# Kernel tuning notes

Hardware: AMD Instinct MI355X
Metric: run time of the kernel (lower is better)

## Reference

```python
import jax, jax.numpy as jnp
import numpy as np

EPS_RMS = 1e-6
EPS_Q = 1e-5


def rmsnorm(x, g):
    var = jnp.mean(x * x, axis=-1, keepdims=True)
    return g * (x * jax.lax.rsqrt(var + EPS_RMS))


def activation_quant(x):
    # per-token 8-bit fake quant with straight-through estimator
    scale = 127.0 / jnp.clip(jnp.max(jnp.abs(x), axis=-1, keepdims=True), EPS_Q)
    y = jnp.clip(jnp.round(x * scale), -128, 127) / scale
    return x + jax.lax.stop_gradient(y - x)


def weight_quant(w):
    # per-tensor ternary fake quant with straight-through estimator
    s = jnp.clip(jnp.mean(jnp.abs(w)), EPS_Q)
    y = jnp.clip(jnp.round(w / s), -1, 1) * s
    return w + jax.lax.stop_gradient(y - w)


def bitlinear(x, w, g):
    xq = activation_quant(rmsnorm(x, g))
    wq = weight_quant(w)
    return jnp.einsum('btc,oc->bto', xq, wq)


def setup_inputs() -> dict:
    key = jax.random.key(0)
    ks = jax.random.split(key, 5)
    B, T, C = 2, 2048, 1024
    std = 1.0 / np.sqrt(C)
    inp = {
        'x': jax.random.normal(ks[0], (B, T, C), jnp.float32),
        'wq': jax.random.normal(ks[1], (C, C), jnp.float32) * std,
        'wk': jax.random.normal(ks[2], (C, C), jnp.float32) * std,
        'wv': jax.random.normal(ks[3], (C, C), jnp.float32) * std,
        'wo': jax.random.normal(ks[4], (C, C), jnp.float32) * std,
        'gq': jnp.ones((C,), jnp.float32),
        'gk': jnp.ones((C,), jnp.float32),
        'gv': jnp.ones((C,), jnp.float32),
        'go': jnp.ones((C,), jnp.float32),
    }
    return inp


def reference(x, wq, wk, wv, wo, gq, gk, gv, go):
    B, T, C = x.shape
    n_head = 16
    head_dim = C // n_head

    q = bitlinear(x, wq, gq).reshape(B, T, n_head, head_dim).transpose(0, 2, 1, 3)
    k = bitlinear(x, wk, gk).reshape(B, T, n_head, head_dim).transpose(0, 2, 1, 3)
    v = bitlinear(x, wv, gv).reshape(B, T, n_head, head_dim).transpose(0, 2, 1, 3)

    att = jnp.einsum('bhqd,bhkd->bhqk', q, k) * (1.0 / np.sqrt(head_dim))
    causal = jnp.tril(jnp.ones((T, T), dtype=bool))  # [T,T]
    att = jnp.where(causal[None, None], att, -jnp.inf)
    att = jax.nn.softmax(att, axis=-1)

    y = jnp.einsum('bhqk,bhkd->bhqd', att, v)
    y = y.transpose(0, 2, 1, 3).reshape(B, T, C)
    return bitlinear(y, wo, go)
```

## Files before the change

kernel.cpp:

```cpp
#include <hip/hip_runtime.h>
#include <hip/hip_bf16.h>


typedef __attribute__((ext_vector_type(8))) short bf16x8;
typedef __attribute__((ext_vector_type(4))) float f32x4;
typedef __attribute__((ext_vector_type(4))) int i32x4;

__device__ __forceinline__ f32x4 mfma16(bf16x8 a, bf16x8 b, f32x4 c) {
    return __builtin_amdgcn_mfma_f32_16x16x32_bf16(a, b, c, 0, 0, 0);
}

__device__ __forceinline__ i32x4 mfma_i8(i32x4 a, i32x4 b, i32x4 c) {
    return __builtin_amdgcn_mfma_i32_16x16x64_i8(a, b, c, 0, 0, 0);
}

__device__ __forceinline__ unsigned short f2bf(float f) {
    unsigned int u = __float_as_uint(f);
    unsigned int r = (u + 0x7fffu + ((u >> 16) & 1u)) >> 16;
    return (unsigned short)r;
}

__device__ __forceinline__ unsigned int cvtpk_bf16(float lo, float hi) {
    unsigned int r;
    asm("v_cvt_pk_bf16_f32 %0, %1, %2" : "=v"(r) : "v"(lo), "v"(hi));
    return r;
}

__device__ __forceinline__ float exp2_fast(float x) {
    float r;
    asm("v_exp_f32 %0, %1" : "=v"(r) : "v"(x));
    return r;
}

__device__ __forceinline__ void gload_lds16(const void* g, void* l) {
    __builtin_amdgcn_global_load_lds((const __attribute__((address_space(1))) unsigned int*)g,
                                     (__attribute__((address_space(3))) unsigned int*)l, 16, 0, 0);
}

__device__ __forceinline__ int pack4i8(float a, float b, float c, float d) {
    unsigned int u = ((unsigned int)((int)a & 255)) | (((unsigned int)((int)b & 255)) << 8) |
                     (((unsigned int)((int)c & 255)) << 16) | (((unsigned int)((int)d & 255)) << 24);
    return (int)u;
}

__device__ __forceinline__ float wredsum(float v) {
#pragma unroll
    for (int o = 32; o > 0; o >>= 1) v += __shfl_xor(v, o);
    return v;
}
__device__ __forceinline__ float wredmax(float v) {
#pragma unroll
    for (int o = 32; o > 0; o >>= 1) v = fmaxf(v, __shfl_xor(v, o));
    return v;
}

__global__ __launch_bounds__(256) void wabssum(const float* __restrict__ w0, const float* __restrict__ w1,
                                               const float* __restrict__ w2, const float* __restrict__ w3,
                                               float* __restrict__ part) {
    int widx = blockIdx.x >> 5, b = blockIdx.x & 31;
    const float* w = (widx == 0) ? w0 : (widx == 1) ? w1 : (widx == 2) ? w2 : w3;
    const float4* w4 = (const float4*)w;
    int tid = threadIdx.x;
    float s = 0.f;
    int base = b * 8192 + tid;
#pragma unroll
    for (int i = 0; i < 32; ++i) {
        float4 v = w4[base + i * 256];
        s += fabsf(v.x) + fabsf(v.y) + fabsf(v.z) + fabsf(v.w);
    }
    s = wredsum(s);
    __shared__ float red[4];
    int wid = tid >> 6, lid = tid & 63;
    if (lid == 0) red[wid] = s;
    __syncthreads();
    if (tid == 0) part[blockIdx.x] = red[0] + red[1] + red[2] + red[3];
}

__global__ __launch_bounds__(256) void wquant(const float* __restrict__ w0, const float* __restrict__ w1,
                                              const float* __restrict__ w2, const float* __restrict__ w3,
                                              const float* __restrict__ part, signed char* __restrict__ wq8) {
    int widx = blockIdx.x >> 6, b = blockIdx.x & 63;
    const float* w = (widx == 0) ? w0 : (widx == 1) ? w1 : (widx == 2) ? w2 : w3;
    float s = 0.f;
#pragma unroll
    for (int i = 0; i < 32; ++i) s += part[widx * 32 + i];
    s = fmaxf(s * (1.f / 1048576.f), 1e-5f);
    float inv = 1.f / s;
    const float4* w4 = (const float4*)w;
    int* dst = (int*)(wq8 + (size_t)widx * 1048576);
    int tid = threadIdx.x;
#pragma unroll
    for (int it = 0; it < 16; ++it) {
        int i4 = b * 4096 + it * 256 + tid;
        float4 v = w4[i4];
        float q0 = fminf(fmaxf(rintf(v.x * inv), -1.f), 1.f);
        float q1 = fminf(fmaxf(rintf(v.y * inv), -1.f), 1.f);
        float q2 = fminf(fmaxf(rintf(v.z * inv), -1.f), 1.f);
        float q3 = fminf(fmaxf(rintf(v.w * inv), -1.f), 1.f);
        dst[i4] = pack4i8(q0, q1, q2, q3);
    }
}

template <int NP>
__global__ __launch_bounds__(256) void actquant(const float* __restrict__ x, const float* __restrict__ g0,
                                                const float* __restrict__ g1, const float* __restrict__ g2,
                                                signed char* __restrict__ aq, float* __restrict__ ascale) {
    int m = blockIdx.x, tid = threadIdx.x;
    int wid = tid >> 6, lid = tid & 63;
    __shared__ float red[4];
    float4 xv = ((const float4*)(x + (size_t)m * 1024))[tid];
    float ss = xv.x * xv.x + xv.y * xv.y + xv.z * xv.z + xv.w * xv.w;
    ss = wredsum(ss);
    if (lid == 0) red[wid] = ss;
    __syncthreads();
    float rstd = rsqrtf((red[0] + red[1] + red[2] + red[3]) * (1.f / 1024.f) + 1e-6f);
    const float* gs[3] = {g0, g1, g2};
#pragma unroll
    for (int p = 0; p < NP; ++p) {
        float4 gv = ((const float4*)gs[p])[tid];
        float a0 = xv.x * gv.x * rstd, a1 = xv.y * gv.y * rstd;
        float a2 = xv.z * gv.z * rstd, a3 = xv.w * gv.w * rstd;
        float am = fmaxf(fmaxf(fabsf(a0), fabsf(a1)), fmaxf(fabsf(a2), fabsf(a3)));
        am = wredmax(am);
        __syncthreads();
        if (lid == 0) red[wid] = am;
        __syncthreads();
        float rm = fmaxf(fmaxf(red[0], red[1]), fmaxf(red[2], red[3]));
        float scale = 127.f / fmaxf(rm, 1e-5f);
        float q0 = fminf(fmaxf(rintf(a0 * scale), -128.f), 127.f);
        float q1 = fminf(fmaxf(rintf(a1 * scale), -128.f), 127.f);
        float q2 = fminf(fmaxf(rintf(a2 * scale), -128.f), 127.f);
        float q3 = fminf(fmaxf(rintf(a3 * scale), -128.f), 127.f);
        ((int*)(aq + (size_t)p * 4194304 + (size_t)m * 1024))[tid] = pack4i8(q0, q1, q2, q3);
        if (tid == 0) ascale[p * 4096 + m] = scale;
    }
}

template <int MODE>
__device__ __forceinline__ void gemm_core(const signed char* __restrict__ A,
                                          const float* __restrict__ asc,
                                          const signed char* __restrict__ W, float s_w,
                                          void* __restrict__ outp, int bm, int bn,
                                          char* As, char* Bs) {
    int tid = threadIdx.x;
    int w = tid >> 6, l = tid & 63;
    int wr = w >> 1, wc = w & 1;
    int lr = l & 15, lh = l >> 4;
    i32x4 acc[4][4] = {};
    int srow = l >> 3;
    int scolb = (((l & 7) ^ srow)) * 16;
    int key16 = (lr & 7) * 16;
    const signed char* Ab = A + (size_t)(bm * 128) * 1024;
    const signed char* Wb = W + (size_t)(bn * 128) * 1024;

    auto STAGE = [&](int kt, int buf) {
        int k0 = kt * 128;
        char* Ad = As + buf * 16384;
        char* Bd = Bs + buf * 16384;
#pragma unroll
        for (int j = 0; j < 4; ++j) {
            int c = j * 4 + w;
            gload_lds16(Ab + (size_t)(c * 8 + srow) * 1024 + k0 + scolb, Ad + c * 1024);
            gload_lds16(Wb + (size_t)(c * 8 + srow) * 1024 + k0 + scolb, Bd + c * 1024);
        }
    };

    STAGE(0, 0);
    __syncthreads();
    for (int kt = 0; kt < 8; ++kt) {
        int cur = kt & 1;
        if (kt < 7) STAGE(kt + 1, cur ^ 1);
        const char* Ar = As + cur * 16384;
        const char* Br = Bs + cur * 16384;
#pragma unroll
        for (int ks = 0; ks < 2; ++ks) {
            int kb = (ks * 64 + lh * 16) ^ key16;
            i32x4 af[4], bfr[4];
#pragma unroll
            for (int mi = 0; mi < 4; ++mi) af[mi] = *(const i32x4*)&Ar[(wr * 64 + mi * 16 + lr) * 128 + kb];
#pragma unroll
            for (int ni = 0; ni < 4; ++ni) bfr[ni] = *(const i32x4*)&Br[(wc * 64 + ni * 16 + lr) * 128 + kb];
#pragma unroll
            for (int mi = 0; mi < 4; ++mi)
#pragma unroll
                for (int ni = 0; ni < 4; ++ni) acc[mi][ni] = mfma_i8(af[mi], bfr[ni], acc[mi][ni]);
        }
        __syncthreads();
    }
#pragma unroll
    for (int mi = 0; mi < 4; ++mi) {
        int mbase = bm * 128 + wr * 64 + mi * 16 + lh * 4;
#pragma unroll
        for (int ni = 0; ni < 4; ++ni) {
            int n = bn * 128 + wc * 64 + ni * 16 + lr;
            if (MODE == 1) {
                int b = mbase >> 11, t0 = mbase & 2047;
                int h = n >> 6, d = n & 63;
                ushort4 st;
                st.x = f2bf((float)acc[mi][ni][0] * s_w / asc[mbase + 0]);
                st.y = f2bf((float)acc[mi][ni][1] * s_w / asc[mbase + 1]);
                st.z = f2bf((float)acc[mi][ni][2] * s_w / asc[mbase + 2]);
                st.w = f2bf((float)acc[mi][ni][3] * s_w / asc[mbase + 3]);
                *(ushort4*)&((unsigned short*)outp)[(size_t)(b * 16 + h) * 131072 + (size_t)d * 2048 + t0] = st;
            } else {
#pragma unroll
                for (int i = 0; i < 4; ++i) {
                    int m = mbase + i;
                    float val = (float)acc[mi][ni][i] * s_w / asc[m];
                    if (MODE == 0) {
                        int b = m >> 11, t = m & 2047, h = n >> 6, d = n & 63;
                        ((unsigned short*)outp)[(size_t)(b * 16 + h) * 131072 + (size_t)t * 64 + d] = f2bf(val);
                    } else {
                        ((float*)outp)[(size_t)m * 1024 + n] = val;
                    }
                }
            }
        }
    }
}

__device__ __forceinline__ float sw_from_part(const float* part) {
    float s = 0.f;
#pragma unroll
    for (int i = 0; i < 32; ++i) s += part[i];
    return fmaxf(s * (1.f / 1048576.f), 1e-5f);
}

__global__ __launch_bounds__(256) void gemm_qkv(const signed char* __restrict__ abf,
                                                const float* __restrict__ ascale,
                                                const signed char* __restrict__ wq8,
                                                const float* __restrict__ part,
                                                unsigned short* __restrict__ qbf,
                                                unsigned short* __restrict__ kbf,
                                                unsigned short* __restrict__ vtb) {
    __shared__ alignas(16) char As[32768];
    __shared__ alignas(16) char Bs[32768];
    int z = blockIdx.z;
    const signed char* A = abf + (size_t)z * 4194304;
    const float* asc = ascale + z * 4096;
    const signed char* W = wq8 + (size_t)z * 1048576;
    float s_w = sw_from_part(part + z * 32);
    int bm = blockIdx.x, bn = blockIdx.y;
    if (z == 0) {
        gemm_core<0>(A, asc, W, s_w, qbf, bm, bn, As, Bs);
    } else if (z == 1) {
        gemm_core<0>(A, asc, W, s_w, kbf, bm, bn, As, Bs);
    } else {
        gemm_core<1>(A, asc, W, s_w, vtb, bm, bn, As, Bs);
    }
}

__global__ __launch_bounds__(256) void gemm_o(const signed char* __restrict__ A,
                                              const float* __restrict__ asc,
                                              const signed char* __restrict__ W,
                                              const float* __restrict__ part, float* __restrict__ outp) {
    __shared__ alignas(16) char As[32768];
    __shared__ alignas(16) char Bs[32768];
    float s_w = sw_from_part(part);
    gemm_core<2>(A, asc, W, s_w, outp, blockIdx.x, blockIdx.y, As, Bs);
}

__global__ __launch_bounds__(64) void attn(const unsigned short* __restrict__ qb,
                                           const unsigned short* __restrict__ kb,
                                           const unsigned short* __restrict__ vt, float* __restrict__ y) {
    int blk = blockIdx.x;
    int bh = blk & 31;
    int c = 63 - (blk >> 5);
    int q0 = c << 5;
    int l = threadIdx.x & 63;
    int lr = l & 15, lh = l >> 4;
    const unsigned short* qbase = qb + (size_t)bh * 131072;
    const unsigned short* kbase = kb + (size_t)bh * 131072;
    const unsigned short* vbase = vt + (size_t)bh * 131072;

    bf16x8 qf00 = *(const bf16x8*)&qbase[(size_t)(q0 + lr) * 64 + lh * 8];
    bf16x8 qf01 = *(const bf16x8*)&qbase[(size_t)(q0 + lr) * 64 + 32 + lh * 8];
    bf16x8 qf10 = *(const bf16x8*)&qbase[(size_t)(q0 + 16 + lr) * 64 + lh * 8];
    bf16x8 qf11 = *(const bf16x8*)&qbase[(size_t)(q0 + 16 + lr) * 64 + 32 + lh * 8];

    f32x4 o[4][2] = {};
    const float ninf = -__builtin_inff();
    const float SC = 0.125f * 1.44269504f;
    float mreg0 = ninf, mreg1 = ninf;
    float lreg0 = 0.f, lreg1 = 0.f;
    __shared__ alignas(16) unsigned short plds[2][16][40];

    int qrow0 = q0 + lr, qrow1 = q0 + 16 + lr;
    int ntiles = c + 1;

    auto LOADK = [&](int kv0, bf16x8* k) {
        k[0] = *(const bf16x8*)&kbase[(size_t)(kv0 + lr) * 64 + lh * 8];
        k[1] = *(const bf16x8*)&kbase[(size_t)(kv0 + lr) * 64 + 32 + lh * 8];
        k[2] = *(const bf16x8*)&kbase[(size_t)(kv0 + 16 + lr) * 64 + lh * 8];
        k[3] = *(const bf16x8*)&kbase[(size_t)(kv0 + 16 + lr) * 64 + 32 + lh * 8];
    };
    auto LOADV = [&](int kv0, bf16x8* v) {
        v[0] = *(const bf16x8*)&vbase[(size_t)(lr)*2048 + kv0 + lh * 8];
        v[1] = *(const bf16x8*)&vbase[(size_t)(16 + lr) * 2048 + kv0 + lh * 8];
        v[2] = *(const bf16x8*)&vbase[(size_t)(32 + lr) * 2048 + kv0 + lh * 8];
        v[3] = *(const bf16x8*)&vbase[(size_t)(48 + lr) * 2048 + kv0 + lh * 8];
    };
    auto PROCESS = [&](int t, bf16x8* k, bf16x8* v) {
        int kv0 = t << 5;
        __builtin_amdgcn_s_setprio(1);
        f32x4 s00 = {}, s01 = {}, s10 = {}, s11 = {};
        s00 = mfma16(k[0], qf00, s00);
        s00 = mfma16(k[1], qf01, s00);
        s01 = mfma16(k[2], qf00, s01);
        s01 = mfma16(k[3], qf01, s01);
        s10 = mfma16(k[0], qf10, s10);
        s10 = mfma16(k[1], qf11, s10);
        s11 = mfma16(k[2], qf10, s11);
        s11 = mfma16(k[3], qf11, s11);
        __builtin_amdgcn_s_setprio(0);
        float p0[8], p1[8];
        if (t == c) {
#pragma unroll
            for (int r = 0; r < 4; ++r) {
                int kva = kv0 + lh * 4 + r, kvb = kv0 + 16 + lh * 4 + r;
                p0[r]     = (kva <= qrow0) ? s00[r] * SC : ninf;
                p0[r + 4] = (kvb <= qrow0) ? s01[r] * SC : ninf;
                p1[r]     = (kva <= qrow1) ? s10[r] * SC : ninf;
                p1[r + 4] = (kvb <= qrow1) ? s11[r] * SC : ninf;
            }
        } else {
#pragma unroll
            for (int r = 0; r < 4; ++r) {
                p0[r] = s00[r] * SC;
                p0[r + 4] = s01[r] * SC;
                p1[r] = s10[r] * SC;
                p1[r + 4] = s11[r] * SC;
            }
        }
        float t0 = fmaxf(fmaxf(fmaxf(p0[0], p0[1]), fmaxf(p0[2], p0[3])),
                         fmaxf(fmaxf(p0[4], p0[5]), fmaxf(p0[6], p0[7])));
        float t1 = fmaxf(fmaxf(fmaxf(p1[0], p1[1]), fmaxf(p1[2], p1[3])),
                         fmaxf(fmaxf(p1[4], p1[5]), fmaxf(p1[6], p1[7])));
        t0 = fmaxf(t0, __shfl_xor(t0, 16));
        t0 = fmaxf(t0, __shfl_xor(t0, 32));
        t1 = fmaxf(t1, __shfl_xor(t1, 16));
        t1 = fmaxf(t1, __shfl_xor(t1, 32));
        if (__any((t0 > mreg0 + 11.f) || (t1 > mreg1 + 11.f))) {
            float mn0 = fmaxf(mreg0, t0), mn1 = fmaxf(mreg1, t1);
            float cc0 = exp2_fast(mreg0 - mn0), cc1 = exp2_fast(mreg1 - mn1);
            lreg0 *= cc0;
            lreg1 *= cc1;
            mreg0 = mn0;
            mreg1 = mn1;
#pragma unroll
            for (int dt = 0; dt < 4; ++dt)
#pragma unroll
                for (int r = 0; r < 4; ++r) {
                    o[dt][0][r] *= cc0;
                    o[dt][1][r] *= cc1;
                }
        }
        float ps0[8], ps1[8];
#pragma unroll
        for (int r = 0; r < 8; ++r) {
            ps0[r] = exp2_fast(p0[r] - mreg0);
            ps1[r] = exp2_fast(p1[r] - mreg1);
        }
        float sum0 = ((ps0[0] + ps0[1]) + (ps0[2] + ps0[3])) + ((ps0[4] + ps0[5]) + (ps0[6] + ps0[7]));
        float sum1 = ((ps1[0] + ps1[1]) + (ps1[2] + ps1[3])) + ((ps1[4] + ps1[5]) + (ps1[6] + ps1[7]));
        sum0 += __shfl_xor(sum0, 16);
        sum0 += __shfl_xor(sum0, 32);
        sum1 += __shfl_xor(sum1, 16);
        sum1 += __shfl_xor(sum1, 32);
        lreg0 += sum0;
        lreg1 += sum1;
        uint2 w0lo, w0hi, w1lo, w1hi;
        w0lo.x = cvtpk_bf16(ps0[0], ps0[1]);
        w0lo.y = cvtpk_bf16(ps0[2], ps0[3]);
        w0hi.x = cvtpk_bf16(ps0[4], ps0[5]);
        w0hi.y = cvtpk_bf16(ps0[6], ps0[7]);
        w1lo.x = cvtpk_bf16(ps1[0], ps1[1]);
        w1lo.y = cvtpk_bf16(ps1[2], ps1[3]);
        w1hi.x = cvtpk_bf16(ps1[4], ps1[5]);
        w1hi.y = cvtpk_bf16(ps1[6], ps1[7]);
        *(uint2*)&plds[0][lr][lh * 4] = w0lo;
        *(uint2*)&plds[0][lr][16 + lh * 4] = w0hi;
        *(uint2*)&plds[1][lr][lh * 4] = w1lo;
        *(uint2*)&plds[1][lr][16 + lh * 4] = w1hi;
        bf16x8 pf0 = *(const bf16x8*)&plds[0][lr][lh * 8];
        bf16x8 pf1 = *(const bf16x8*)&plds[1][lr][lh * 8];
        __builtin_amdgcn_s_setprio(1);
#pragma unroll
        for (int dt = 0; dt < 4; ++dt) {
            o[dt][0] = mfma16(v[dt], pf0, o[dt][0]);
            o[dt][1] = mfma16(v[dt], pf1, o[dt][1]);
        }
        __builtin_amdgcn_s_setprio(0);
    };

    bf16x8 kA[4], vA[4], kB[4], vB[4];
    LOADK(0, kA);
    LOADV(0, vA);
    int t = 0;
    while (true) {
        if (t + 1 < ntiles) { LOADK((t + 1) << 5, kB); LOADV((t + 1) << 5, vB); }
        PROCESS(t, kA, vA);
        if (++t >= ntiles) break;
        if (t + 1 < ntiles) { LOADK((t + 1) << 5, kA); LOADV((t + 1) << 5, vA); }
        PROCESS(t, kB, vB);
        if (++t >= ntiles) break;
    }

    int b = bh >> 4, h = bh & 15;
#pragma unroll
    for (int qt = 0; qt < 2; ++qt) {
        int qrow = (qt == 0) ? qrow0 : qrow1;
        float invl = 1.f / ((qt == 0) ? lreg0 : lreg1);
        float* yr = y + (size_t)(b * 2048 + qrow) * 1024 + h * 64;
#pragma unroll
        for (int dt = 0; dt < 4; ++dt) {
            float4 st;
            st.x = o[dt][qt][0] * invl;
            st.y = o[dt][qt][1] * invl;
            st.z = o[dt][qt][2] * invl;
            st.w = o[dt][qt][3] * invl;
            *(float4*)&yr[dt * 16 + lh * 4] = st;
        }
    }
}

extern "C" void kernel_launch(void* const* d_in, const int* in_sizes, int n_in,
                              void* d_out, int out_size, void* d_ws, size_t ws_size,
                              hipStream_t stream) {
    const float* x  = (const float*)d_in[0];
    const float* wq = (const float*)d_in[1];
    const float* wk = (const float*)d_in[2];
    const float* wv = (const float*)d_in[3];
    const float* wo = (const float*)d_in[4];
    const float* gq = (const float*)d_in[5];
    const float* gk = (const float*)d_in[6];
    const float* gv = (const float*)d_in[7];
    const float* go = (const float*)d_in[8];

    char* ws = (char*)d_ws;
    size_t off = 0;
    auto alloc = [&](size_t bytes) {
        size_t o = off;
        off += (bytes + 255) & ~(size_t)255;
        return o;
    };
    float* part = (float*)(ws + alloc(128 * 4));
    signed char* wq8 = (signed char*)(ws + alloc(4ull * 1048576));
    signed char* abf = (signed char*)(ws + alloc(3ull * 4194304));
    float* asc = (float*)(ws + alloc(3ull * 4096 * 4));
    unsigned short* qbf = (unsigned short*)(ws + alloc(4194304ull * 2));
    unsigned short* kbf = (unsigned short*)(ws + alloc(4194304ull * 2));
    unsigned short* vtb = (unsigned short*)(ws + alloc(4194304ull * 2));
    float* ybuf = (float*)(ws + alloc(4194304ull * 4));
    signed char* ybf = (signed char*)(ws + alloc(4194304ull));
    float* ysc = (float*)(ws + alloc(4096 * 4));
    (void)ws_size; (void)in_sizes; (void)n_in; (void)out_size;

    wabssum<<<128, 256, 0, stream>>>(wq, wk, wv, wo, part);
    wquant<<<256, 256, 0, stream>>>(wq, wk, wv, wo, part, wq8);
    actquant<3><<<4096, 256, 0, stream>>>(x, gq, gk, gv, abf, asc);
    gemm_qkv<<<dim3(32, 8, 3), 256, 0, stream>>>(abf, asc, wq8, part, qbf, kbf, vtb);
    attn<<<2048, 64, 0, stream>>>(qbf, kbf, vtb, ybuf);
    actquant<1><<<4096, 256, 0, stream>>>(ybuf, go, go, go, ybf, ysc);
    gemm_o<<<dim3(32, 8), 256, 0, stream>>>(ybf, ysc, wq8 + 3ull * 1048576, part + 96, (float*)d_out);
}
```

Baseline: 144.6 us.

## Split attention KV tiles across four waves with LDS merge of partial softmax

Each attention block now runs four wavefronts that take interleaved KV tiles (stride 4) for the same 32 query rows. Each wave keeps its own online-softmax state, and the partial outputs plus max/sum values are written to shared memory and combined in a log-sum-exp merge before the store. This shortens the serial KV loop per block, which was long for late query chunks and caused load imbalance and low occupancy. In exchange it adds about 32KB of LDS per block, a barrier, and merge arithmetic, and early query chunks leave some waves idle.

```diff
diff --git a/kernel.cpp b/kernel.cpp
--- a/kernel.cpp
+++ b/kernel.cpp
@@ -260,13 +260,14 @@
     gemm_core<2>(A, asc, W, s_w, outp, blockIdx.x, blockIdx.y, As, Bs);
 }
 
-__global__ __launch_bounds__(64) void attn(const unsigned short* __restrict__ qb,
-                                           const unsigned short* __restrict__ kb,
-                                           const unsigned short* __restrict__ vt, float* __restrict__ y) {
+__global__ __launch_bounds__(256) void attn(const unsigned short* __restrict__ qb,
+                                            const unsigned short* __restrict__ kb,
+                                            const unsigned short* __restrict__ vt, float* __restrict__ y) {
     int blk = blockIdx.x;
     int bh = blk & 31;
     int c = 63 - (blk >> 5);
     int q0 = c << 5;
+    int w = threadIdx.x >> 6;
     int l = threadIdx.x & 63;
     int lr = l & 15, lh = l >> 4;
     const unsigned short* qbase = qb + (size_t)bh * 131072;
@@ -283,10 +284,11 @@
     const float SC = 0.125f * 1.44269504f;
     float mreg0 = ninf, mreg1 = ninf;
     float lreg0 = 0.f, lreg1 = 0.f;
-    __shared__ alignas(16) unsigned short plds[2][16][40];
+    __shared__ alignas(16) unsigned short plds[4][2][16][40];
+    __shared__ alignas(16) float om[4][32][64];
+    __shared__ float mlm[4][2][32];
 
     int qrow0 = q0 + lr, qrow1 = q0 + 16 + lr;
-    int ntiles = c + 1;
 
     auto LOADK = [&](int kv0, bf16x8* k) {
         k[0] = *(const bf16x8*)&kbase[(size_t)(kv0 + lr) * 64 + lh * 8];
@@ -378,12 +380,12 @@
         w1lo.y = cvtpk_bf16(ps1[2], ps1[3]);
         w1hi.x = cvtpk_bf16(ps1[4], ps1[5]);
         w1hi.y = cvtpk_bf16(ps1[6], ps1[7]);
-        *(uint2*)&plds[0][lr][lh * 4] = w0lo;
-        *(uint2*)&plds[0][lr][16 + lh * 4] = w0hi;
-        *(uint2*)&plds[1][lr][lh * 4] = w1lo;
-        *(uint2*)&plds[1][lr][16 + lh * 4] = w1hi;
-        bf16x8 pf0 = *(const bf16x8*)&plds[0][lr][lh * 8];
-        bf16x8 pf1 = *(const bf16x8*)&plds[1][lr][lh * 8];
+        *(uint2*)&plds[w][0][lr][lh * 4] = w0lo;
+        *(uint2*)&plds[w][0][lr][16 + lh * 4] = w0hi;
+        *(uint2*)&plds[w][1][lr][lh * 4] = w1lo;
+        *(uint2*)&plds[w][1][lr][16 + lh * 4] = w1hi;
+        bf16x8 pf0 = *(const bf16x8*)&plds[w][0][lr][lh * 8];
+        bf16x8 pf1 = *(const bf16x8*)&plds[w][1][lr][lh * 8];
         __builtin_amdgcn_s_setprio(1);
 #pragma unroll
         for (int dt = 0; dt < 4; ++dt) {
@@ -393,34 +395,59 @@
         __builtin_amdgcn_s_setprio(0);
     };
 
-    bf16x8 kA[4], vA[4], kB[4], vB[4];
-    LOADK(0, kA);
-    LOADV(0, vA);
-    int t = 0;
-    while (true) {
-        if (t + 1 < ntiles) { LOADK((t + 1) << 5, kB); LOADV((t + 1) << 5, vB); }
-        PROCESS(t, kA, vA);
-        if (++t >= ntiles) break;
-        if (t + 1 < ntiles) { LOADK((t + 1) << 5, kA); LOADV((t + 1) << 5, vA); }
-        PROCESS(t, kB, vB);
-        if (++t >= ntiles) break;
-    }
-
+    int t = w;
+    if (t <= c) {
+        bf16x8 kA[4], vA[4], kB[4], vB[4];
+        LOADK(t << 5, kA);
+        LOADV(t << 5, vA);
+        while (true) {
+            if (t + 4 <= c) { LOADK((t + 4) << 5, kB); LOADV((t + 4) << 5, vB); }
+            PROCESS(t, kA, vA);
+            t += 4;
+            if (t > c) break;
+            if (t + 4 <= c) { LOADK((t + 4) << 5, kA); LOADV((t + 4) << 5, vA); }
+            PROCESS(t, kB, vB);
+            t += 4;
+            if (t > c) break;
+        }
+    }
+
+#pragma unroll
+    for (int dt = 0; dt < 4; ++dt) {
+        *(float4*)&om[w][lr][dt * 16 + lh * 4] = *(float4*)&o[dt][0];
+        *(float4*)&om[w][16 + lr][dt * 16 + lh * 4] = *(float4*)&o[dt][1];
+    }
+    if (lh == 0) {
+        mlm[w][0][lr] = mreg0;
+        mlm[w][1][lr] = lreg0;
+        mlm[w][0][16 + lr] = mreg1;
+        mlm[w][1][16 + lr] = lreg1;
+    }
+    __syncthreads();
+
+    int tid = threadIdx.x;
+    int row = tid >> 3;
+    int d0 = (tid & 7) * 8;
+    float m0 = mlm[0][0][row], m1 = mlm[1][0][row], m2 = mlm[2][0][row], m3 = mlm[3][0][row];
+    float ms = fmaxf(fmaxf(m0, m1), fmaxf(m2, m3));
+    float s0 = exp2_fast(m0 - ms), s1 = exp2_fast(m1 - ms);
+    float s2 = exp2_fast(m2 - ms), s3 = exp2_fast(m3 - ms);
+    float lt = mlm[0][1][row] * s0 + mlm[1][1][row] * s1 + mlm[2][1][row] * s2 + mlm[3][1][row] * s3;
+    float invl = 1.f / lt;
     int b = bh >> 4, h = bh & 15;
-#pragma unroll
-    for (int qt = 0; qt < 2; ++qt) {
-        int qrow = (qt == 0) ? qrow0 : qrow1;
-        float invl = 1.f / ((qt == 0) ? lreg0 : lreg1);
-        float* yr = y + (size_t)(b * 2048 + qrow) * 1024 + h * 64;
-#pragma unroll
-        for (int dt = 0; dt < 4; ++dt) {
-            float4 st;
-            st.x = o[dt][qt][0] * invl;
-            st.y = o[dt][qt][1] * invl;
-            st.z = o[dt][qt][2] * invl;
-            st.w = o[dt][qt][3] * invl;
-            *(float4*)&yr[dt * 16 + lh * 4] = st;
-        }
+    float* yr = y + (size_t)(b * 2048 + q0 + row) * 1024 + h * 64 + d0;
+#pragma unroll
+    for (int j = 0; j < 8; j += 4) {
+        float4 v0 = *(float4*)&om[0][row][d0 + j];
+        float4 v1 = *(float4*)&om[1][row][d0 + j];
+        float4 v2 = *(float4*)&om[2][row][d0 + j];
+        float4 v3 = *(float4*)&om[3][row][d0 + j];
+        float4 st;
+        st.x = (v0.x * s0 + v1.x * s1 + v2.x * s2 + v3.x * s3) * invl;
+        st.y = (v0.y * s0 + v1.y * s1 + v2.y * s2 + v3.y * s3) * invl;
+        st.z = (v0.z * s0 + v1.z * s1 + v2.z * s2 + v3.z * s3) * invl;
+        st.w = (v0.w * s0 + v1.w * s1 + v2.w * s2 + v3.w * s3) * invl;
+        *(float4*)&yr[j] = st;
     }
 }
 
@@ -460,7 +487,7 @@
     wquant<<<256, 256, 0, stream>>>(wq, wk, wv, wo, part, wq8);
     actquant<3><<<4096, 256, 0, stream>>>(x, gq, gk, gv, abf, asc);
     gemm_qkv<<<dim3(32, 8, 3), 256, 0, stream>>>(abf, asc, wq8, part, qbf, kbf, vtb);
-    attn<<<2048, 64, 0, stream>>>(qbf, kbf, vtb, ybuf);
+    attn<<<2048, 256, 0, stream>>>(qbf, kbf, vtb, ybuf);
     actquant<1><<<4096, 256, 0, stream>>>(ybuf, go, go, go, ybf, ysc);
     gemm_o<<<dim3(32, 8), 256, 0, stream>>>(ybf, ysc, wq8 + 3ull * 1048576, part + 96, (float*)d_out);
 }
```

Result: no change. 144.5 us (-0.1%).

## Share K/V tiles across four attention waves via swizzled LDS double buffering

Applied to the files above, without the earlier changes.

The attention kernel now runs four waves per block, each owning a 32-row query chunk of a 128-row group. K and V tiles are staged cooperatively into XOR-swizzled LDS with global-to-LDS loads and double-buffered, so each tile is fetched once per block instead of once per wave. This cuts global and L2 traffic but adds a __syncthreads per tile. Waves with fewer causal tiles sit idle until the block's last wave finishes, and the grid drops to 512 blocks.

```diff
diff --git a/kernel.cpp b/kernel.cpp
--- a/kernel.cpp
+++ b/kernel.cpp
@@ -260,18 +260,22 @@
     gemm_core<2>(A, asc, W, s_w, outp, blockIdx.x, blockIdx.y, As, Bs);
 }
 
-__global__ __launch_bounds__(64) void attn(const unsigned short* __restrict__ qb,
-                                           const unsigned short* __restrict__ kb,
-                                           const unsigned short* __restrict__ vt, float* __restrict__ y) {
+__global__ __launch_bounds__(256) void attn(const unsigned short* __restrict__ qb,
+                                            const unsigned short* __restrict__ kb,
+                                            const unsigned short* __restrict__ vt, float* __restrict__ y) {
     int blk = blockIdx.x;
     int bh = blk & 31;
-    int c = 63 - (blk >> 5);
-    int q0 = c << 5;
+    int g = 15 - (blk >> 5);
+    int w = threadIdx.x >> 6;
     int l = threadIdx.x & 63;
     int lr = l & 15, lh = l >> 4;
+    int cw = 4 * g + w;
+    int q0 = cw << 5;
+    int NT = 4 * g + 4;
+
     const unsigned short* qbase = qb + (size_t)bh * 131072;
-    const unsigned short* kbase = kb + (size_t)bh * 131072;
-    const unsigned short* vbase = vt + (size_t)bh * 131072;
+    const char* kbytes = (const char*)(kb + (size_t)bh * 131072);
+    const char* vbytes = (const char*)(vt + (size_t)bh * 131072);
 
     bf16x8 qf00 = *(const bf16x8*)&qbase[(size_t)(q0 + lr) * 64 + lh * 8];
     bf16x8 qf01 = *(const bf16x8*)&qbase[(size_t)(q0 + lr) * 64 + 32 + lh * 8];
@@ -283,38 +287,42 @@
     const float SC = 0.125f * 1.44269504f;
     float mreg0 = ninf, mreg1 = ninf;
     float lreg0 = 0.f, lreg1 = 0.f;
-    __shared__ alignas(16) unsigned short plds[2][16][40];
+
+    __shared__ alignas(16) char Ks[2][4096];
+    __shared__ alignas(16) char Vs[2][4096];
+    __shared__ alignas(16) unsigned short plds[4][2][16][40];
 
     int qrow0 = q0 + lr, qrow1 = q0 + 16 + lr;
-    int ntiles = c + 1;
-
-    auto LOADK = [&](int kv0, bf16x8* k) {
-        k[0] = *(const bf16x8*)&kbase[(size_t)(kv0 + lr) * 64 + lh * 8];
-        k[1] = *(const bf16x8*)&kbase[(size_t)(kv0 + lr) * 64 + 32 + lh * 8];
-        k[2] = *(const bf16x8*)&kbase[(size_t)(kv0 + 16 + lr) * 64 + lh * 8];
-        k[3] = *(const bf16x8*)&kbase[(size_t)(kv0 + 16 + lr) * 64 + 32 + lh * 8];
+
+    auto STAGE = [&](int t, int buf) {
+        int kv0 = t << 5;
+        gload_lds16(kbytes + (size_t)(kv0 + w * 8 + (l >> 3)) * 128 + (((l & 7) ^ (l >> 3)) * 16),
+                    &Ks[buf][w * 1024]);
+        gload_lds16(vbytes + (size_t)(w * 16 + (l >> 2)) * 4096 + (size_t)kv0 * 2 +
+                        (((l & 3) ^ ((l >> 2) & 3)) * 16),
+                    &Vs[buf][w * 1024]);
     };
-    auto LOADV = [&](int kv0, bf16x8* v) {
-        v[0] = *(const bf16x8*)&vbase[(size_t)(lr)*2048 + kv0 + lh * 8];
-        v[1] = *(const bf16x8*)&vbase[(size_t)(16 + lr) * 2048 + kv0 + lh * 8];
-        v[2] = *(const bf16x8*)&vbase[(size_t)(32 + lr) * 2048 + kv0 + lh * 8];
-        v[3] = *(const bf16x8*)&vbase[(size_t)(48 + lr) * 2048 + kv0 + lh * 8];
-    };
-    auto PROCESS = [&](int t, bf16x8* k, bf16x8* v) {
+
+    auto PROCESS = [&](int t, const char* Kb, const char* Vb) {
         int kv0 = t << 5;
+        int k7 = lr & 7;
+        bf16x8 k0 = *(const bf16x8*)(Kb + lr * 128 + ((lh ^ k7) * 16));
+        bf16x8 k1 = *(const bf16x8*)(Kb + lr * 128 + (((4 + lh) ^ k7) * 16));
+        bf16x8 k2 = *(const bf16x8*)(Kb + (16 + lr) * 128 + ((lh ^ k7) * 16));
+        bf16x8 k3 = *(const bf16x8*)(Kb + (16 + lr) * 128 + (((4 + lh) ^ k7) * 16));
         __builtin_amdgcn_s_setprio(1);
         f32x4 s00 = {}, s01 = {}, s10 = {}, s11 = {};
-        s00 = mfma16(k[0], qf00, s00);
-        s00 = mfma16(k[1], qf01, s00);
-        s01 = mfma16(k[2], qf00, s01);
-        s01 = mfma16(k[3], qf01, s01);
-        s10 = mfma16(k[0], qf10, s10);
-        s10 = mfma16(k[1], qf11, s10);
-        s11 = mfma16(k[2], qf10, s11);
-        s11 = mfma16(k[3], qf11, s11);
+        s00 = mfma16(k0, qf00, s00);
+        s00 = mfma16(k1, qf01, s00);
+        s01 = mfma16(k2, qf00, s01);
+        s01 = mfma16(k3, qf01, s01);
+        s10 = mfma16(k0, qf10, s10);
+        s10 = mfma16(k1, qf11, s10);
+        s11 = mfma16(k2, qf10, s11);
+        s11 = mfma16(k3, qf11, s11);
         __builtin_amdgcn_s_setprio(0);
         float p0[8], p1[8];
-        if (t == c) {
+        if (t == cw) {
 #pragma unroll
             for (int r = 0; r < 4; ++r) {
                 int kva = kv0 + lh * 4 + r, kvb = kv0 + 16 + lh * 4 + r;
@@ -378,32 +386,30 @@
         w1lo.y = cvtpk_bf16(ps1[2], ps1[3]);
         w1hi.x = cvtpk_bf16(ps1[4], ps1[5]);
         w1hi.y = cvtpk_bf16(ps1[6], ps1[7]);
-        *(uint2*)&plds[0][lr][lh * 4] = w0lo;
-        *(uint2*)&plds[0][lr][16 + lh * 4] = w0hi;
-        *(uint2*)&plds[1][lr][lh * 4] = w1lo;
-        *(uint2*)&plds[1][lr][16 + lh * 4] = w1hi;
-        bf16x8 pf0 = *(const bf16x8*)&plds[0][lr][lh * 8];
-        bf16x8 pf1 = *(const bf16x8*)&plds[1][lr][lh * 8];
+        *(uint2*)&plds[w][0][lr][lh * 4] = w0lo;
+        *(uint2*)&plds[w][0][lr][16 + lh * 4] = w0hi;
+        *(uint2*)&plds[w][1][lr][lh * 4] = w1lo;
+        *(uint2*)&plds[w][1][lr][16 + lh * 4] = w1hi;
+        bf16x8 pf0 = *(const bf16x8*)&plds[w][0][lr][lh * 8];
+        bf16x8 pf1 = *(const bf16x8*)&plds[w][1][lr][lh * 8];
         __builtin_amdgcn_s_setprio(1);
 #pragma unroll
         for (int dt = 0; dt < 4; ++dt) {
-            o[dt][0] = mfma16(v[dt], pf0, o[dt][0]);
-            o[dt][1] = mfma16(v[dt], pf1, o[dt][1]);
+            int d = dt * 16 + lr;
+            bf16x8 vv = *(const bf16x8*)(Vb + d * 64 + ((lh ^ (lr & 3)) * 16));
+            o[dt][0] = mfma16(vv, pf0, o[dt][0]);
+            o[dt][1] = mfma16(vv, pf1, o[dt][1]);
         }
         __builtin_amdgcn_s_setprio(0);
     };
 
-    bf16x8 kA[4], vA[4], kB[4], vB[4];
-    LOADK(0, kA);
-    LOADV(0, vA);
-    int t = 0;
-    while (true) {
-        if (t + 1 < ntiles) { LOADK((t + 1) << 5, kB); LOADV((t + 1) << 5, vB); }
-        PROCESS(t, kA, vA);
-        if (++t >= ntiles) break;
-        if (t + 1 < ntiles) { LOADK((t + 1) << 5, kA); LOADV((t + 1) << 5, vA); }
-        PROCESS(t, kB, vB);
-        if (++t >= ntiles) break;
+    STAGE(0, 0);
+    __syncthreads();
+    for (int t = 0; t < NT; ++t) {
+        int buf = t & 1;
+        if (t + 1 < NT) STAGE(t + 1, buf ^ 1);
+        if (t <= cw) PROCESS(t, Ks[buf], Vs[buf]);
+        __syncthreads();
     }
 
     int b = bh >> 4, h = bh & 15;
@@ -460,7 +466,7 @@
     wquant<<<256, 256, 0, stream>>>(wq, wk, wv, wo, part, wq8);
     actquant<3><<<4096, 256, 0, stream>>>(x, gq, gk, gv, abf, asc);
     gemm_qkv<<<dim3(32, 8, 3), 256, 0, stream>>>(abf, asc, wq8, part, qbf, kbf, vtb);
-    attn<<<2048, 64, 0, stream>>>(qbf, kbf, vtb, ybuf);
+    attn<<<512, 256, 0, stream>>>(qbf, kbf, vtb, ybuf);
     actquant<1><<<4096, 256, 0, stream>>>(ybuf, go, go, go, ybf, ysc);
     gemm_o<<<dim3(32, 8), 256, 0, stream>>>(ybf, ysc, wq8 + 3ull * 1048576, part + 96, (float*)d_out);
 }
```

Result: no change. 146.6 us (+1.4%).

## Double attention query tile per wave to 64 rows to reuse K/V loads

Applied to the files above, without the earlier changes.

Each single-wave attention block now processes 64 query rows (four 16-row sub-tiles) instead of 32, halving the grid to 1024 blocks. Every K and V fragment loaded from global memory is reused across four query sub-tiles, halving K/V traffic per query. The causal mask now applies to the last two KV tiles. In exchange, register pressure rises (16 accumulators, 8 Q fragments), which may lower occupancy, and there are fewer blocks to balance the causal workload.

```diff
diff --git a/kernel.cpp b/kernel.cpp
--- a/kernel.cpp
+++ b/kernel.cpp
@@ -265,28 +265,29 @@
                                            const unsigned short* __restrict__ vt, float* __restrict__ y) {
     int blk = blockIdx.x;
     int bh = blk & 31;
-    int c = 63 - (blk >> 5);
-    int q0 = c << 5;
+    int c = 31 - (blk >> 5);
+    int q0 = c << 6;
+    int c2 = c << 1;
+    int ntiles = c2 + 2;
     int l = threadIdx.x & 63;
     int lr = l & 15, lh = l >> 4;
     const unsigned short* qbase = qb + (size_t)bh * 131072;
     const unsigned short* kbase = kb + (size_t)bh * 131072;
     const unsigned short* vbase = vt + (size_t)bh * 131072;
 
-    bf16x8 qf00 = *(const bf16x8*)&qbase[(size_t)(q0 + lr) * 64 + lh * 8];
-    bf16x8 qf01 = *(const bf16x8*)&qbase[(size_t)(q0 + lr) * 64 + 32 + lh * 8];
-    bf16x8 qf10 = *(const bf16x8*)&qbase[(size_t)(q0 + 16 + lr) * 64 + lh * 8];
-    bf16x8 qf11 = *(const bf16x8*)&qbase[(size_t)(q0 + 16 + lr) * 64 + 32 + lh * 8];
-
-    f32x4 o[4][2] = {};
+    bf16x8 qf[4][2];
+#pragma unroll
+    for (int qt = 0; qt < 4; ++qt) {
+        qf[qt][0] = *(const bf16x8*)&qbase[(size_t)(q0 + qt * 16 + lr) * 64 + lh * 8];
+        qf[qt][1] = *(const bf16x8*)&qbase[(size_t)(q0 + qt * 16 + lr) * 64 + 32 + lh * 8];
+    }
+
+    f32x4 o[4][4] = {};
     const float ninf = -__builtin_inff();
     const float SC = 0.125f * 1.44269504f;
-    float mreg0 = ninf, mreg1 = ninf;
-    float lreg0 = 0.f, lreg1 = 0.f;
-    __shared__ alignas(16) unsigned short plds[2][16][40];
-
-    int qrow0 = q0 + lr, qrow1 = q0 + 16 + lr;
-    int ntiles = c + 1;
+    float ml[4] = {ninf, ninf, ninf, ninf};
+    float ls[4] = {0.f, 0.f, 0.f, 0.f};
+    __shared__ alignas(16) unsigned short plds[4][16][40];
 
     auto LOADK = [&](int kv0, bf16x8* k) {
         k[0] = *(const bf16x8*)&kbase[(size_t)(kv0 + lr) * 64 + lh * 8];
@@ -300,95 +301,86 @@
         v[2] = *(const bf16x8*)&vbase[(size_t)(32 + lr) * 2048 + kv0 + lh * 8];
         v[3] = *(const bf16x8*)&vbase[(size_t)(48 + lr) * 2048 + kv0 + lh * 8];
     };
+
     auto PROCESS = [&](int t, bf16x8* k, bf16x8* v) {
         int kv0 = t << 5;
+        float p[4][8];
         __builtin_amdgcn_s_setprio(1);
-        f32x4 s00 = {}, s01 = {}, s10 = {}, s11 = {};
-        s00 = mfma16(k[0], qf00, s00);
-        s00 = mfma16(k[1], qf01, s00);
-        s01 = mfma16(k[2], qf00, s01);
-        s01 = mfma16(k[3], qf01, s01);
-        s10 = mfma16(k[0], qf10, s10);
-        s10 = mfma16(k[1], qf11, s10);
-        s11 = mfma16(k[2], qf10, s11);
-        s11 = mfma16(k[3], qf11, s11);
+#pragma unroll
+        for (int qt = 0; qt < 4; ++qt) {
+            f32x4 sa = {}, sb = {};
+            sa = mfma16(k[0], qf[qt][0], sa);
+            sa = mfma16(k[1], qf[qt][1], sa);
+            sb = mfma16(k[2], qf[qt][0], sb);
+            sb = mfma16(k[3], qf[qt][1], sb);
+#pragma unroll
+            for (int r = 0; r < 4; ++r) {
+                p[qt][r] = sa[r] * SC;
+                p[qt][r + 4] = sb[r] * SC;
+            }
+        }
         __builtin_amdgcn_s_setprio(0);
-        float p0[8], p1[8];
-        if (t == c) {
-#pragma unroll
-            for (int r = 0; r < 4; ++r) {
-                int kva = kv0 + lh * 4 + r, kvb = kv0 + 16 + lh * 4 + r;
-                p0[r]     = (kva <= qrow0) ? s00[r] * SC : ninf;
-                p0[r + 4] = (kvb <= qrow0) ? s01[r] * SC : ninf;
-                p1[r]     = (kva <= qrow1) ? s10[r] * SC : ninf;
-                p1[r + 4] = (kvb <= qrow1) ? s11[r] * SC : ninf;
+        if (t >= c2) {
+#pragma unroll
+            for (int qt = 0; qt < 4; ++qt) {
+                int qrow = q0 + qt * 16 + lr;
+#pragma unroll
+                for (int r = 0; r < 4; ++r) {
+                    if (kv0 + lh * 4 + r > qrow) p[qt][r] = ninf;
+                    if (kv0 + 16 + lh * 4 + r > qrow) p[qt][r + 4] = ninf;
+                }
             }
-        } else {
-#pragma unroll
-            for (int r = 0; r < 4; ++r) {
-                p0[r] = s00[r] * SC;
-                p0[r + 4] = s01[r] * SC;
-                p1[r] = s10[r] * SC;
-                p1[r + 4] = s11[r] * SC;
+        }
+        float tm[4];
+#pragma unroll
+        for (int qt = 0; qt < 4; ++qt) {
+            float tq = fmaxf(fmaxf(fmaxf(p[qt][0], p[qt][1]), fmaxf(p[qt][2], p[qt][3])),
+                             fmaxf(fmaxf(p[qt][4], p[qt][5]), fmaxf(p[qt][6], p[qt][7])));
+            tq = fmaxf(tq, __shfl_xor(tq, 16));
+            tq = fmaxf(tq, __shfl_xor(tq, 32));
+            tm[qt] = tq;
+        }
+        bool need = (tm[0] > ml[0] + 11.f) || (tm[1] > ml[1] + 11.f) ||
+                    (tm[2] > ml[2] + 11.f) || (tm[3] > ml[3] + 11.f);
+        if (__any(need)) {
+#pragma unroll
+            for (int qt = 0; qt < 4; ++qt) {
+                float mn = fmaxf(ml[qt], tm[qt]);
+                float cc = exp2_fast(ml[qt] - mn);
+                ls[qt] *= cc;
+                ml[qt] = mn;
+#pragma unroll
+                for (int dt = 0; dt < 4; ++dt)
+#pragma unroll
+                    for (int r = 0; r < 4; ++r) o[dt][qt][r] *= cc;
             }
         }
-        float t0 = fmaxf(fmaxf(fmaxf(p0[0], p0[1]), fmaxf(p0[2], p0[3])),
-                         fmaxf(fmaxf(p0[4], p0[5]), fmaxf(p0[6], p0[7])));
-        float t1 = fmaxf(fmaxf(fmaxf(p1[0], p1[1]), fmaxf(p1[2], p1[3])),
-                         fmaxf(fmaxf(p1[4], p1[5]), fmaxf(p1[6], p1[7])));
-        t0 = fmaxf(t0, __shfl_xor(t0, 16));
-        t0 = fmaxf(t0, __shfl_xor(t0, 32));
-        t1 = fmaxf(t1, __shfl_xor(t1, 16));
-        t1 = fmaxf(t1, __shfl_xor(t1, 32));
-        if (__any((t0 > mreg0 + 11.f) || (t1 > mreg1 + 11.f))) {
-            float mn0 = fmaxf(mreg0, t0), mn1 = fmaxf(mreg1, t1);
-            float cc0 = exp2_fast(mreg0 - mn0), cc1 = exp2_fast(mreg1 - mn1);
-            lreg0 *= cc0;
-            lreg1 *= cc1;
-            mreg0 = mn0;
-            mreg1 = mn1;
-#pragma unroll
-            for (int dt = 0; dt < 4; ++dt)
-#pragma unroll
-                for (int r = 0; r < 4; ++r) {
-                    o[dt][0][r] *= cc0;
-                    o[dt][1][r] *= cc1;
-                }
-        }
-        float ps0[8], ps1[8];
-#pragma unroll
-        for (int r = 0; r < 8; ++r) {
-            ps0[r] = exp2_fast(p0[r] - mreg0);
-            ps1[r] = exp2_fast(p1[r] - mreg1);
-        }
-        float sum0 = ((ps0[0] + ps0[1]) + (ps0[2] + ps0[3])) + ((ps0[4] + ps0[5]) + (ps0[6] + ps0[7]));
-        float sum1 = ((ps1[0] + ps1[1]) + (ps1[2] + ps1[3])) + ((ps1[4] + ps1[5]) + (ps1[6] + ps1[7]));
-        sum0 += __shfl_xor(sum0, 16);
-        sum0 += __shfl_xor(sum0, 32);
-        sum1 += __shfl_xor(sum1, 16);
-        sum1 += __shfl_xor(sum1, 32);
-        lreg0 += sum0;
-        lreg1 += sum1;
-        uint2 w0lo, w0hi, w1lo, w1hi;
-        w0lo.x = cvtpk_bf16(ps0[0], ps0[1]);
-        w0lo.y = cvtpk_bf16(ps0[2], ps0[3]);
-        w0hi.x = cvtpk_bf16(ps0[4], ps0[5]);
-        w0hi.y = cvtpk_bf16(ps0[6], ps0[7]);
-        w1lo.x = cvtpk_bf16(ps1[0], ps1[1]);
-        w1lo.y = cvtpk_bf16(ps1[2], ps1[3]);
-        w1hi.x = cvtpk_bf16(ps1[4], ps1[5]);
-        w1hi.y = cvtpk_bf16(ps1[6], ps1[7]);
-        *(uint2*)&plds[0][lr][lh * 4] = w0lo;
-        *(uint2*)&plds[0][lr][16 + lh * 4] = w0hi;
-        *(uint2*)&plds[1][lr][lh * 4] = w1lo;
-        *(uint2*)&plds[1][lr][16 + lh * 4] = w1hi;
-        bf16x8 pf0 = *(const bf16x8*)&plds[0][lr][lh * 8];
-        bf16x8 pf1 = *(const bf16x8*)&plds[1][lr][lh * 8];
+#pragma unroll
+        for (int qt = 0; qt < 4; ++qt) {
+            float ps[8];
+#pragma unroll
+            for (int r = 0; r < 8; ++r) ps[r] = exp2_fast(p[qt][r] - ml[qt]);
+            float sum = ((ps[0] + ps[1]) + (ps[2] + ps[3])) + ((ps[4] + ps[5]) + (ps[6] + ps[7]));
+            sum += __shfl_xor(sum, 16);
+            sum += __shfl_xor(sum, 32);
+            ls[qt] += sum;
+            uint2 wlo, whi;
+            wlo.x = cvtpk_bf16(ps[0], ps[1]);
+            wlo.y = cvtpk_bf16(ps[2], ps[3]);
+            whi.x = cvtpk_bf16(ps[4], ps[5]);
+            whi.y = cvtpk_bf16(ps[6], ps[7]);
+            *(uint2*)&plds[qt][lr][lh * 4] = wlo;
+            *(uint2*)&plds[qt][lr][16 + lh * 4] = whi;
+        }
+        bf16x8 pf[4];
+#pragma unroll
+        for (int qt = 0; qt < 4; ++qt) pf[qt] = *(const bf16x8*)&plds[qt][lr][lh * 8];
         __builtin_amdgcn_s_setprio(1);
 #pragma unroll
         for (int dt = 0; dt < 4; ++dt) {
-            o[dt][0] = mfma16(v[dt], pf0, o[dt][0]);
-            o[dt][1] = mfma16(v[dt], pf1, o[dt][1]);
+            bf16x8 vv = v[dt];
+#pragma unroll
+            for (int qt = 0; qt < 4; ++qt) o[dt][qt] = mfma16(vv, pf[qt], o[dt][qt]);
         }
         __builtin_amdgcn_s_setprio(0);
     };
@@ -408,9 +400,9 @@
 
     int b = bh >> 4, h = bh & 15;
 #pragma unroll
-    for (int qt = 0; qt < 2; ++qt) {
-        int qrow = (qt == 0) ? qrow0 : qrow1;
-        float invl = 1.f / ((qt == 0) ? lreg0 : lreg1);
+    for (int qt = 0; qt < 4; ++qt) {
+        int qrow = q0 + qt * 16 + lr;
+        float invl = 1.f / ls[qt];
         float* yr = y + (size_t)(b * 2048 + qrow) * 1024 + h * 64;
 #pragma unroll
         for (int dt = 0; dt < 4; ++dt) {
@@ -460,7 +452,7 @@
     wquant<<<256, 256, 0, stream>>>(wq, wk, wv, wo, part, wq8);
     actquant<3><<<4096, 256, 0, stream>>>(x, gq, gk, gv, abf, asc);
     gemm_qkv<<<dim3(32, 8, 3), 256, 0, stream>>>(abf, asc, wq8, part, qbf, kbf, vtb);
-    attn<<<2048, 64, 0, stream>>>(qbf, kbf, vtb, ybuf);
+    attn<<<1024, 64, 0, stream>>>(qbf, kbf, vtb, ybuf);
     actquant<1><<<4096, 256, 0, stream>>>(ybuf, go, go, go, ybf, ysc);
     gemm_o<<<dim3(32, 8), 256, 0, stream>>>(ybf, ysc, wq8 + 3ull * 1048576, part + 96, (float*)d_out);
 }
```

New measurement: 168.2 us. 1.16x slower.
